# Performance work log

Measured on AMD Instinct MI355X. Metric: run time of the kernel, lower is better.

Reference implementation:

```python
import jax, jax.numpy as jnp
import numpy as np

L = 10      # LSTM layers
H = 128     # hidden size
ENC = 4096  # traffic_encoder_output_len
B = 8192    # batch
T = 12      # points_to_predict
NUM_MODES = 25


def setup_inputs() -> dict:
    key = jax.random.key(0)
    ks = jax.random.split(key, 10)
    s = 1.0 / np.sqrt(H)
    return {
        "backbone_encoded": jax.random.normal(ks[0], (B, ENC), jnp.float32),
        "fc_in_W": jax.random.normal(ks[1], (H, ENC), jnp.float32) / np.sqrt(ENC),
        "fc_in_b": jax.random.normal(ks[2], (H,), jnp.float32) * s,
        "Wih": jax.random.normal(ks[3], (L, 4 * H, H), jnp.float32) * s,
        "Whh": jax.random.normal(ks[4], (L, 4 * H, H), jnp.float32) * s,
        "bih": jax.random.normal(ks[5], (L, 4 * H), jnp.float32) * s,
        "bhh": jax.random.normal(ks[6], (L, 4 * H), jnp.float32) * s,
        "fc_out_W": jax.random.normal(ks[7], (3 * NUM_MODES, H), jnp.float32) * s,
        "fc_out_b": jax.random.normal(ks[8], (3 * NUM_MODES,), jnp.float32) * s,
        "points_to_predict": T,
    }


def _lstm_stack(x, Wih, Whh, bih, bhh):
    # x: [B, T, H]; PyTorch gate order: i, f, g, o
    def run_layer(x, l):
        def step(carry, xt):
            h, c = carry
            gates = xt @ Wih[l].T + h @ Whh[l].T + bih[l] + bhh[l]  # [B, 4H]
            i, f, g, o = jnp.split(gates, 4, axis=-1)
            c = jax.nn.sigmoid(f) * c + jax.nn.sigmoid(i) * jnp.tanh(g)
            h = jax.nn.sigmoid(o) * jnp.tanh(c)
            return (h, c), h
        b = x.shape[0]
        h0 = jnp.zeros((b, H), x.dtype)
        _, ys = jax.lax.scan(step, (h0, h0), jnp.swapaxes(x, 0, 1))  # [T, B, H]
        return jnp.swapaxes(ys, 0, 1)

    for l in range(L):
        x = run_layer(x, l)
    return x


def reference(backbone_encoded, fc_in_W, fc_in_b, Wih, Whh, bih, bhh,
              fc_out_W, fc_out_b, points_to_predict):
    enc = jax.nn.relu(backbone_encoded @ fc_in_W.T + fc_in_b)        # [B, H]
    x = jnp.repeat(enc[:, None, :], points_to_predict, axis=1)      # [B, T, H]
    y = _lstm_stack(x, Wih, Whh, bih, bhh)                           # [B, T, H]
    fc = y @ fc_out_W.T + fc_out_b                                   # [B, T, 75]
    b, t, _ = fc.shape
    # chunk(25, dim=channels) of consecutive pairs -> [B, 25, T, 2]
    predictions = fc[:, :, :50].reshape(b, t, NUM_MODES, 2).transpose(0, 2, 1, 3)
    probabilities = jax.nn.softmax(fc[:, -1, 50:], axis=-1)          # [B, 25]
    return predictions, probabilities
```

## Files before the change

kernel.cpp:

```cpp
#include <hip/hip_runtime.h>

typedef _Float16 h16;
typedef _Float16 h4 __attribute__((ext_vector_type(4)));
typedef _Float16 h8 __attribute__((ext_vector_type(8)));
typedef float f4 __attribute__((ext_vector_type(4)));

#define NB 8192
#define NENC 4096
#define NH 128
#define NL 10
#define NT 12
#define PAD 136

#define OFF_FCIN 0
#define SZ_FCIN (128*4096)
#define OFF_W (OFF_FCIN + SZ_FCIN)
#define SZ_W (10*2*512*128)
#define OFF_FCOUT (OFF_W + SZ_W)
#define SZ_FCOUT (80*128)
#define OFF_ENC (OFF_FCOUT + SZ_FCOUT)
#define SZ_ENC (8192*128)
#define OFF_GX0 (OFF_ENC + SZ_ENC)
#define SZ_GX0 (8192*512)
#define BYTE_BIAS ((OFF_GX0 + SZ_GX0)*2)

__device__ __forceinline__ float sigf(float x) {
  float e = __builtin_amdgcn_exp2f(-1.4426950408889634f * x);
  return __builtin_amdgcn_rcpf(1.0f + e);
}
__device__ __forceinline__ float tanhf_(float x) {
  float e = __builtin_amdgcn_exp2f(-2.8853900817779268f * x);
  return 2.0f * __builtin_amdgcn_rcpf(1.0f + e) - 1.0f;
}
__device__ __forceinline__ f4 splat4(float v) { f4 r; r[0]=v; r[1]=v; r[2]=v; r[3]=v; return r; }
__device__ __forceinline__ h8 cvt8(float4 a, float4 b) {
  h8 r; r[0]=(h16)a.x; r[1]=(h16)a.y; r[2]=(h16)a.z; r[3]=(h16)a.w;
  r[4]=(h16)b.x; r[5]=(h16)b.y; r[6]=(h16)b.z; r[7]=(h16)b.w; return r;
}

__global__ __launch_bounds__(256) void prep(const float* __restrict__ fcinW,
                                            const float* __restrict__ Wih,
                                            const float* __restrict__ Whh,
                                            const float* __restrict__ bih,
                                            const float* __restrict__ bhh,
                                            const float* __restrict__ fcoutW,
                                            h16* __restrict__ wsh,
                                            float* __restrict__ wbias) {
  int idx = blockIdx.x * 256 + threadIdx.x;
  if (idx < 65536) {
    int r = idx >> 9, k8 = idx & 511;
    const float* src = fcinW + r * 4096 + k8 * 8;
    h8 v = cvt8(*(const float4*)src, *(const float4*)(src + 4));
    *(h8*)(wsh + OFF_FCIN + (((r >> 4) * 512 + k8) * 128 + (r & 15) * 8)) = v;
  } else if (idx < 229376) {
    int rel = idx - 65536;
    int l = rel >> 14, rr = rel & 16383;
    int ssel = rr >> 13, rk8 = rr & 8191;
    int r = rk8 >> 4, k8 = rk8 & 15;
    const float* src = (ssel ? Whh : Wih) + l * 65536 + r * 128 + k8 * 8;
    h8 v = cvt8(*(const float4*)src, *(const float4*)(src + 4));
    *(h8*)(wsh + OFF_W + (l * 2 + ssel) * 65536 +
           (((r >> 4) * 16 + k8) * 128 + (r & 15) * 8)) = v;
  } else if (idx < 230656) {
    int rel = idx - 229376;
    int r = rel >> 4, k8 = rel & 15;
    h8 v;
    if (r < 75) {
      const float* src = fcoutW + r * 128 + k8 * 8;
      v = cvt8(*(const float4*)src, *(const float4*)(src + 4));
    } else {
      for (int j = 0; j < 8; ++j) v[j] = (h16)0.f;
    }
    *(h8*)(wsh + OFF_FCOUT + (((r >> 4) * 16 + k8) * 128 + (r & 15) * 8)) = v;
  } else if (idx < 235776) {
    int rel = idx - 230656;
    wbias[rel] = bih[rel] + bhh[rel];
  }
}

__global__ __launch_bounds__(256) void kin(const float* __restrict__ A,
                                           const float* __restrict__ bvec,
                                           h16* __restrict__ wsh) {
  const h16* Wp = wsh + OFF_FCIN;
  h16* ench = wsh + OFF_ENC;
  int tid = threadIdx.x;
  int w = tid >> 6, lane = tid & 63, s = lane & 15, q = lane >> 4;
  int m0 = blockIdx.x * 16;
  int c0 = w * 32 + s, c1 = c0 + 16;
  f4 acc0 = splat4(bvec[c0]);
  f4 acc1 = splat4(bvec[c1]);
  const float* arow = A + (size_t)(m0 + s) * NENC;
  const h16* wp0 = Wp + (w * 2 + 0) * (512 * 128) + s * 8;
  const h16* wp1 = Wp + (w * 2 + 1) * (512 * 128) + s * 8;
#pragma unroll 4
  for (int kb = 0; kb < 128; ++kb) {
    int k0 = kb * 32 + q * 8;
    float4 x0 = *(const float4*)(arow + k0);
    float4 x1 = *(const float4*)(arow + k0 + 4);
    h8 af = cvt8(x0, x1);
    h8 b0 = *(const h8*)(wp0 + (kb * 4 + q) * 128);
    h8 b1 = *(const h8*)(wp1 + (kb * 4 + q) * 128);
    acc0 = __builtin_amdgcn_mfma_f32_16x16x32_f16(af, b0, acc0, 0, 0, 0);
    acc1 = __builtin_amdgcn_mfma_f32_16x16x32_f16(af, b1, acc1, 0, 0, 0);
  }
#pragma unroll
  for (int r = 0; r < 4; ++r) {
    int b = m0 + q * 4 + r;
    float v0 = acc0[r]; v0 = v0 > 0.f ? v0 : 0.f;
    float v1 = acc1[r]; v1 = v1 > 0.f ? v1 : 0.f;
    ench[(size_t)b * NH + c0] = (h16)v0;
    ench[(size_t)b * NH + c1] = (h16)v1;
  }
}

__global__ __launch_bounds__(256) void kin2(h16* __restrict__ wsh,
                                            const float* __restrict__ wbias) {
  int tid = threadIdx.x;
  int w2 = tid >> 6, lane = tid & 63, s = lane & 15, q = lane >> 4;
  int bid = blockIdx.x;
  int lb = bid >> 3, mt = (bid >> 2) & 1, cg = bid & 3;
  const h16* ench = wsh + OFF_ENC;
  const h16* wih0 = wsh + OFF_W;
  h16* gx0 = wsh + OFF_GX0;
  const h16* arow = ench + (size_t)(lb * 32 + mt * 16 + s) * NH;
  h8 ax[4];
#pragma unroll
  for (int kt = 0; kt < 4; ++kt) ax[kt] = *(const h8*)(arow + kt * 32 + q * 8);
#pragma unroll
  for (int ti = 0; ti < 2; ++ti) {
    int W = w2 * 2 + ti;
    int rb = cg * 8 + W;
    f4 acc = splat4(wbias[cg * 128 + W * 16 + s]);
#pragma unroll
    for (int kt = 0; kt < 4; ++kt) {
      h8 b = *(const h8*)(wih0 + (rb * 16 + kt * 4 + q) * 128 + s * 8);
      acc = __builtin_amdgcn_mfma_f32_16x16x32_f16(ax[kt], b, acc, 0, 0, 0);
    }
    h4 st; st[0] = (h16)acc[0]; st[1] = (h16)acc[1]; st[2] = (h16)acc[2]; st[3] = (h16)acc[3];
    *(h4*)(gx0 + ((((size_t)lb * 8 + W) * 8 + cg * 2 + mt) * 64 + lane) * 4) = st;
  }
}

__global__ __launch_bounds__(512, 2) void lstm(h16* __restrict__ wsh,
                                               const float* __restrict__ wbias,
                                               const float* __restrict__ fcoutb,
                                               float* __restrict__ out) {
  __shared__ h16 ring[13][32][PAD];
  __shared__ float probst[32 * 26];
  int tid = threadIdx.x;
  int w = tid >> 6, lane = tid & 63, s = lane & 15, q = lane >> 4;
  int brow = blockIdx.x * 32;
  h8 wx[4][4], wh[4][4];
  float bb[4];
  float c[2][4];

  {
    const h16* whh = wsh + OFF_W + 65536;
#pragma unroll
    for (int g = 0; g < 4; ++g)
#pragma unroll
      for (int kt = 0; kt < 4; ++kt)
        wh[g][kt] = *(const h8*)(whh + (((g * 8 + w) * 16 + kt * 4 + q) * 128) + s * 8);
    f4 gx[4][2];
    const h16* gxp = wsh + OFF_GX0 + ((size_t)blockIdx.x * 8 + w) * 8 * 256 + (size_t)lane * 4;
#pragma unroll
    for (int g = 0; g < 4; ++g)
#pragma unroll
      for (int mt = 0; mt < 2; ++mt) {
        h4 v = *(const h4*)(gxp + (g * 2 + mt) * 256);
        f4 a; a[0] = (float)v[0]; a[1] = (float)v[1]; a[2] = (float)v[2]; a[3] = (float)v[3];
        gx[g][mt] = a;
      }
#pragma unroll
    for (int mt = 0; mt < 2; ++mt)
#pragma unroll
      for (int r = 0; r < 4; ++r) c[mt][r] = 0.f;
    for (int t = 0; t < NT; ++t) {
      __syncthreads();
      int rw = t + 11; if (rw >= 13) rw -= 13;
      int rh = t + 10; if (rh >= 13) rh -= 13;
      f4 acc[4][2];
#pragma unroll
      for (int g = 0; g < 4; ++g)
#pragma unroll
        for (int mt = 0; mt < 2; ++mt) acc[g][mt] = gx[g][mt];
      if (t > 0) {
#pragma unroll
        for (int mt = 0; mt < 2; ++mt) {
          h8 ah[4];
#pragma unroll
          for (int kt = 0; kt < 4; ++kt)
            ah[kt] = *(const h8*)&ring[rh][mt * 16 + s][kt * 32 + q * 8];
#pragma unroll
          for (int g = 0; g < 4; ++g)
#pragma unroll
            for (int kt = 0; kt < 4; ++kt)
              acc[g][mt] = __builtin_amdgcn_mfma_f32_16x16x32_f16(ah[kt], wh[g][kt], acc[g][mt], 0, 0, 0);
        }
      }
#pragma unroll
      for (int mt = 0; mt < 2; ++mt)
#pragma unroll
        for (int r = 0; r < 4; ++r) {
          float iv = acc[0][mt][r], fv = acc[1][mt][r];
          float gv = acc[2][mt][r], ov = acc[3][mt][r];
          float cc = sigf(fv) * c[mt][r] + sigf(iv) * tanhf_(gv);
          c[mt][r] = cc;
          ring[rw][mt * 16 + q * 4 + r][w * 16 + s] = (h16)(sigf(ov) * tanhf_(cc));
        }
    }
  }
  for (int l = 1; l < NL; ++l) {
    const h16* wih = wsh + OFF_W + (size_t)(l * 2) * 65536;
    const h16* whh = wih + 65536;
#pragma unroll
    for (int g = 0; g < 4; ++g) {
#pragma unroll
      for (int kt = 0; kt < 4; ++kt) {
        int off = (((g * 8 + w) * 16 + kt * 4 + q) * 128) + s * 8;
        wx[g][kt] = *(const h8*)(wih + off);
        wh[g][kt] = *(const h8*)(whh + off);
      }
      bb[g] = wbias[l * 512 + g * 128 + w * 16 + s];
    }
#pragma unroll
    for (int mt = 0; mt < 2; ++mt)
#pragma unroll
      for (int r = 0; r < 4; ++r) c[mt][r] = 0.f;
    int base = 12 - l;
    for (int t = 0; t < NT; ++t) {
      __syncthreads();
      int rr = t + base; if (rr >= 13) rr -= 13;
      int rw = rr - 1; if (rw < 0) rw += 13;
      int rh = rw - 1; if (rh < 0) rh += 13;
      f4 acc[4][2];
#pragma unroll
      for (int g = 0; g < 4; ++g)
#pragma unroll
        for (int mt = 0; mt < 2; ++mt) acc[g][mt] = splat4(bb[g]);
#pragma unroll
      for (int mt = 0; mt < 2; ++mt) {
        h8 ax[4];
#pragma unroll
        for (int kt = 0; kt < 4; ++kt)
          ax[kt] = *(const h8*)&ring[rr][mt * 16 + s][kt * 32 + q * 8];
#pragma unroll
        for (int g = 0; g < 4; ++g)
#pragma unroll
          for (int kt = 0; kt < 4; ++kt)
            acc[g][mt] = __builtin_amdgcn_mfma_f32_16x16x32_f16(ax[kt], wx[g][kt], acc[g][mt], 0, 0, 0);
      }
      if (t > 0) {
#pragma unroll
        for (int mt = 0; mt < 2; ++mt) {
          h8 ah[4];
#pragma unroll
          for (int kt = 0; kt < 4; ++kt)
            ah[kt] = *(const h8*)&ring[rh][mt * 16 + s][kt * 32 + q * 8];
#pragma unroll
          for (int g = 0; g < 4; ++g)
#pragma unroll
            for (int kt = 0; kt < 4; ++kt)
              acc[g][mt] = __builtin_amdgcn_mfma_f32_16x16x32_f16(ah[kt], wh[g][kt], acc[g][mt], 0, 0, 0);
        }
      }
#pragma unroll
      for (int mt = 0; mt < 2; ++mt)
#pragma unroll
        for (int r = 0; r < 4; ++r) {
          float iv = acc[0][mt][r], fv = acc[1][mt][r];
          float gv = acc[2][mt][r], ov = acc[3][mt][r];
          float cc = sigf(fv) * c[mt][r] + sigf(iv) * tanhf_(gv);
          c[mt][r] = cc;
          ring[rw][mt * 16 + q * 4 + r][w * 16 + s] = (h16)(sigf(ov) * tanhf_(cc));
        }
    }
  }
  __syncthreads();
  h8 wo[5][4];
  float bo[5];
  const h16* fco = wsh + OFF_FCOUT;
#pragma unroll
  for (int nt = 0; nt < 5; ++nt) {
#pragma unroll
    for (int kt = 0; kt < 4; ++kt)
      wo[nt][kt] = *(const h8*)(fco + (nt * 16 + kt * 4 + q) * 128 + s * 8);
    int col = nt * 16 + s;
    bo[nt] = (col < 75) ? fcoutb[col] : 0.f;
  }
  int tcount = (w < 4) ? 2 : 1;
  for (int ti = 0; ti < tcount; ++ti) {
    int t = w + ti * 8;
    int sl = t + 2; if (sl >= 13) sl -= 13;
#pragma unroll
    for (int mt = 0; mt < 2; ++mt) {
      h8 ax[4];
#pragma unroll
      for (int kt = 0; kt < 4; ++kt)
        ax[kt] = *(const h8*)&ring[sl][mt * 16 + s][kt * 32 + q * 8];
#pragma unroll
      for (int nt = 0; nt < 5; ++nt) {
        f4 a = splat4(bo[nt]);
#pragma unroll
        for (int kt = 0; kt < 4; ++kt)
          a = __builtin_amdgcn_mfma_f32_16x16x32_f16(ax[kt], wo[nt][kt], a, 0, 0, 0);
        int col = nt * 16 + s;
#pragma unroll
        for (int r = 0; r < 4; ++r) {
          int row = mt * 16 + q * 4 + r;
          int b = brow + row;
          float v = a[r];
          if (col < 50)
            out[(size_t)b * 600 + (col >> 1) * 24 + t * 2 + (col & 1)] = v;
          if (t == 11 && col >= 50 && col < 75)
            probst[row * 26 + (col - 50)] = v;
        }
      }
    }
  }
  __syncthreads();
  if (tid < 32) {
    float vals[25];
    float m = -1e30f;
#pragma unroll
    for (int j = 0; j < 25; ++j) { vals[j] = probst[tid * 26 + j]; m = vals[j] > m ? vals[j] : m; }
    float sum = 0.f;
#pragma unroll
    for (int j = 0; j < 25; ++j) {
      float e = __builtin_amdgcn_exp2f((vals[j] - m) * 1.4426950408889634f);
      vals[j] = e; sum += e;
    }
    float rs = 1.0f / sum;
    size_t pb = (size_t)4915200 + (size_t)(brow + tid) * 25;
#pragma unroll
    for (int j = 0; j < 25; ++j) out[pb + j] = vals[j] * rs;
  }
}

extern "C" void kernel_launch(void* const* d_in, const int* in_sizes, int n_in,
                              void* d_out, int out_size, void* d_ws, size_t ws_size,
                              hipStream_t stream) {
  const float* backbone = (const float*)d_in[0];
  const float* fcinW    = (const float*)d_in[1];
  const float* fcinb    = (const float*)d_in[2];
  const float* Wih      = (const float*)d_in[3];
  const float* Whh      = (const float*)d_in[4];
  const float* bih      = (const float*)d_in[5];
  const float* bhh      = (const float*)d_in[6];
  const float* fcoutW   = (const float*)d_in[7];
  const float* fcoutb   = (const float*)d_in[8];
  h16* wsh = (h16*)d_ws;
  float* wbias = (float*)((char*)d_ws + BYTE_BIAS);

  prep<<<922, 256, 0, stream>>>(fcinW, Wih, Whh, bih, bhh, fcoutW, wsh, wbias);
  kin<<<512, 256, 0, stream>>>(backbone, fcinb, wsh);
  kin2<<<2048, 256, 0, stream>>>(wsh, wbias);
  lstm<<<256, 512, 0, stream>>>(wsh, wbias, fcoutb, (float*)d_out);
}
```

Before: 514.7 us.

## Fuse layer-0 input projection and bias/fc_out prep into LSTM kernel

Removes the separate kin2 kernel that precomputed the layer-0 input gates into a workspace buffer; the LSTM kernel now computes them directly from the encoder output with MFMA. Bias summation and fc_out weight conversion move from prep into the LSTM kernel, and the gate activations are rewritten to share reciprocals (sigmoid*tanh merged into one rcp). The LDS ring padding also changes. This drops a kernel launch and the global round-trip of the gate buffer, at the cost of extra registers and redundant per-block weight conversion.

New measurement: 534.3 us. +3.8%, slower.

```diff
diff --git a/kernel.cpp b/kernel.cpp
--- a/kernel.cpp
+++ b/kernel.cpp
@@ -1,7 +1,6 @@
 #include <hip/hip_runtime.h>
 
 typedef _Float16 h16;
-typedef _Float16 h4 __attribute__((ext_vector_type(4)));
 typedef _Float16 h8 __attribute__((ext_vector_type(8)));
 typedef float f4 __attribute__((ext_vector_type(4)));
 
@@ -10,28 +9,17 @@
 #define NH 128
 #define NL 10
 #define NT 12
-#define PAD 136
+#define PAD 138
 
 #define OFF_FCIN 0
 #define SZ_FCIN (128*4096)
 #define OFF_W (OFF_FCIN + SZ_FCIN)
 #define SZ_W (10*2*512*128)
-#define OFF_FCOUT (OFF_W + SZ_W)
-#define SZ_FCOUT (80*128)
-#define OFF_ENC (OFF_FCOUT + SZ_FCOUT)
+#define OFF_ENC (OFF_W + SZ_W)
 #define SZ_ENC (8192*128)
-#define OFF_GX0 (OFF_ENC + SZ_ENC)
-#define SZ_GX0 (8192*512)
-#define BYTE_BIAS ((OFF_GX0 + SZ_GX0)*2)
-
-__device__ __forceinline__ float sigf(float x) {
-  float e = __builtin_amdgcn_exp2f(-1.4426950408889634f * x);
-  return __builtin_amdgcn_rcpf(1.0f + e);
-}
-__device__ __forceinline__ float tanhf_(float x) {
-  float e = __builtin_amdgcn_exp2f(-2.8853900817779268f * x);
-  return 2.0f * __builtin_amdgcn_rcpf(1.0f + e) - 1.0f;
-}
+
+#define KLOG2 1.4426950408889634f
+
 __device__ __forceinline__ f4 splat4(float v) { f4 r; r[0]=v; r[1]=v; r[2]=v; r[3]=v; return r; }
 __device__ __forceinline__ h8 cvt8(float4 a, float4 b) {
   h8 r; r[0]=(h16)a.x; r[1]=(h16)a.y; r[2]=(h16)a.z; r[3]=(h16)a.w;
@@ -41,11 +29,7 @@
 __global__ __launch_bounds__(256) void prep(const float* __restrict__ fcinW,
                                             const float* __restrict__ Wih,
                                             const float* __restrict__ Whh,
-                                            const float* __restrict__ bih,
-                                            const float* __restrict__ bhh,
-                                            const float* __restrict__ fcoutW,
-                                            h16* __restrict__ wsh,
-                                            float* __restrict__ wbias) {
+                                            h16* __restrict__ wsh) {
   int idx = blockIdx.x * 256 + threadIdx.x;
   if (idx < 65536) {
     int r = idx >> 9, k8 = idx & 511;
@@ -61,20 +45,6 @@
     h8 v = cvt8(*(const float4*)src, *(const float4*)(src + 4));
     *(h8*)(wsh + OFF_W + (l * 2 + ssel) * 65536 +
            (((r >> 4) * 16 + k8) * 128 + (r & 15) * 8)) = v;
-  } else if (idx < 230656) {
-    int rel = idx - 229376;
-    int r = rel >> 4, k8 = rel & 15;
-    h8 v;
-    if (r < 75) {
-      const float* src = fcoutW + r * 128 + k8 * 8;
-      v = cvt8(*(const float4*)src, *(const float4*)(src + 4));
-    } else {
-      for (int j = 0; j < 8; ++j) v[j] = (h16)0.f;
-    }
-    *(h8*)(wsh + OFF_FCOUT + (((r >> 4) * 16 + k8) * 128 + (r & 15) * 8)) = v;
-  } else if (idx < 235776) {
-    int rel = idx - 230656;
-    wbias[rel] = bih[rel] + bhh[rel];
   }
 }
 
@@ -113,36 +83,10 @@
   }
 }
 
-__global__ __launch_bounds__(256) void kin2(h16* __restrict__ wsh,
-                                            const float* __restrict__ wbias) {
-  int tid = threadIdx.x;
-  int w2 = tid >> 6, lane = tid & 63, s = lane & 15, q = lane >> 4;
-  int bid = blockIdx.x;
-  int lb = bid >> 3, mt = (bid >> 2) & 1, cg = bid & 3;
-  const h16* ench = wsh + OFF_ENC;
-  const h16* wih0 = wsh + OFF_W;
-  h16* gx0 = wsh + OFF_GX0;
-  const h16* arow = ench + (size_t)(lb * 32 + mt * 16 + s) * NH;
-  h8 ax[4];
-#pragma unroll
-  for (int kt = 0; kt < 4; ++kt) ax[kt] = *(const h8*)(arow + kt * 32 + q * 8);
-#pragma unroll
-  for (int ti = 0; ti < 2; ++ti) {
-    int W = w2 * 2 + ti;
-    int rb = cg * 8 + W;
-    f4 acc = splat4(wbias[cg * 128 + W * 16 + s]);
-#pragma unroll
-    for (int kt = 0; kt < 4; ++kt) {
-      h8 b = *(const h8*)(wih0 + (rb * 16 + kt * 4 + q) * 128 + s * 8);
-      acc = __builtin_amdgcn_mfma_f32_16x16x32_f16(ax[kt], b, acc, 0, 0, 0);
-    }
-    h4 st; st[0] = (h16)acc[0]; st[1] = (h16)acc[1]; st[2] = (h16)acc[2]; st[3] = (h16)acc[3];
-    *(h4*)(gx0 + ((((size_t)lb * 8 + W) * 8 + cg * 2 + mt) * 64 + lane) * 4) = st;
-  }
-}
-
 __global__ __launch_bounds__(512, 2) void lstm(h16* __restrict__ wsh,
-                                               const float* __restrict__ wbias,
+                                               const float* __restrict__ bih,
+                                               const float* __restrict__ bhh,
+                                               const float* __restrict__ fcoutW,
                                                const float* __restrict__ fcoutb,
                                                float* __restrict__ out) {
   __shared__ h16 ring[13][32][PAD];
@@ -150,27 +94,41 @@
   int tid = threadIdx.x;
   int w = tid >> 6, lane = tid & 63, s = lane & 15, q = lane >> 4;
   int brow = blockIdx.x * 32;
+  const h16* ench = wsh + OFF_ENC;
   h8 wx[4][4], wh[4][4];
-  float bb[4];
   float c[2][4];
 
+  f4 gx[4][2];
   {
-    const h16* whh = wsh + OFF_W + 65536;
-#pragma unroll
-    for (int g = 0; g < 4; ++g)
+    const h16* wih0 = wsh + OFF_W;
+    const h16* whh0 = wih0 + 65536;
+#pragma unroll
+    for (int g = 0; g < 4; ++g) {
+#pragma unroll
+      for (int kt = 0; kt < 4; ++kt) {
+        int off = (((g * 8 + w) * 16 + kt * 4 + q) * 128) + s * 8;
+        wx[g][kt] = *(const h8*)(wih0 + off);
+        wh[g][kt] = *(const h8*)(whh0 + off);
+      }
+      int bcol = g * 128 + w * 16 + s;
+      float bb = bih[bcol] + bhh[bcol];
+#pragma unroll
+      for (int mt = 0; mt < 2; ++mt) gx[g][mt] = splat4(bb);
+    }
+#pragma unroll
+    for (int mt = 0; mt < 2; ++mt) {
+      h8 ax[4];
 #pragma unroll
       for (int kt = 0; kt < 4; ++kt)
-        wh[g][kt] = *(const h8*)(whh + (((g * 8 + w) * 16 + kt * 4 + q) * 128) + s * 8);
-    f4 gx[4][2];
-    const h16* gxp = wsh + OFF_GX0 + ((size_t)blockIdx.x * 8 + w) * 8 * 256 + (size_t)lane * 4;
-#pragma unroll
-    for (int g = 0; g < 4; ++g)
-#pragma unroll
-      for (int mt = 0; mt < 2; ++mt) {
-        h4 v = *(const h4*)(gxp + (g * 2 + mt) * 256);
-        f4 a; a[0] = (float)v[0]; a[1] = (float)v[1]; a[2] = (float)v[2]; a[3] = (float)v[3];
-        gx[g][mt] = a;
-      }
+        ax[kt] = *(const h8*)(ench + (size_t)(brow + mt * 16 + s) * NH + kt * 32 + q * 8);
+#pragma unroll
+      for (int g = 0; g < 4; ++g)
+#pragma unroll
+        for (int kt = 0; kt < 4; ++kt)
+          gx[g][mt] = __builtin_amdgcn_mfma_f32_16x16x32_f16(ax[kt], wx[g][kt], gx[g][mt], 0, 0, 0);
+    }
+  }
+  {
 #pragma unroll
     for (int mt = 0; mt < 2; ++mt)
 #pragma unroll
@@ -203,16 +161,24 @@
 #pragma unroll
         for (int r = 0; r < 4; ++r) {
           float iv = acc[0][mt][r], fv = acc[1][mt][r];
-          float gv = acc[2][mt][r], ov = acc[3][mt][r];
-          float cc = sigf(fv) * c[mt][r] + sigf(iv) * tanhf_(gv);
+          float gv = fmaxf(acc[2][mt][r], -30.f), ov = acc[3][mt][r];
+          float ui = __builtin_amdgcn_exp2f(-KLOG2 * iv);
+          float ug = __builtin_amdgcn_exp2f(-2.f * KLOG2 * gv);
+          float uf = __builtin_amdgcn_exp2f(-KLOG2 * fv);
+          float ig = (1.f - ug) * __builtin_amdgcn_rcpf((1.f + ui) * (1.f + ug));
+          float cc = c[mt][r] * __builtin_amdgcn_rcpf(1.f + uf) + ig;
           c[mt][r] = cc;
-          ring[rw][mt * 16 + q * 4 + r][w * 16 + s] = (h16)(sigf(ov) * tanhf_(cc));
+          float uo = __builtin_amdgcn_exp2f(-KLOG2 * ov);
+          float uc = __builtin_amdgcn_exp2f(-2.f * KLOG2 * cc);
+          float hv = (1.f - uc) * __builtin_amdgcn_rcpf((1.f + uo) * (1.f + uc));
+          ring[rw][mt * 16 + q * 4 + r][w * 16 + s] = (h16)hv;
         }
     }
   }
   for (int l = 1; l < NL; ++l) {
     const h16* wih = wsh + OFF_W + (size_t)(l * 2) * 65536;
     const h16* whh = wih + 65536;
+    float bb[4];
 #pragma unroll
     for (int g = 0; g < 4; ++g) {
 #pragma unroll
@@ -221,7 +187,8 @@
         wx[g][kt] = *(const h8*)(wih + off);
         wh[g][kt] = *(const h8*)(whh + off);
       }
-      bb[g] = wbias[l * 512 + g * 128 + w * 16 + s];
+      int bcol = l * 512 + g * 128 + w * 16 + s;
+      bb[g] = bih[bcol] + bhh[bcol];
     }
 #pragma unroll
     for (int mt = 0; mt < 2; ++mt)
@@ -269,24 +236,37 @@
 #pragma unroll
         for (int r = 0; r < 4; ++r) {
           float iv = acc[0][mt][r], fv = acc[1][mt][r];
-          float gv = acc[2][mt][r], ov = acc[3][mt][r];
-          float cc = sigf(fv) * c[mt][r] + sigf(iv) * tanhf_(gv);
+          float gv = fmaxf(acc[2][mt][r], -30.f), ov = acc[3][mt][r];
+          float ui = __builtin_amdgcn_exp2f(-KLOG2 * iv);
+          float ug = __builtin_amdgcn_exp2f(-2.f * KLOG2 * gv);
+          float uf = __builtin_amdgcn_exp2f(-KLOG2 * fv);
+          float ig = (1.f - ug) * __builtin_amdgcn_rcpf((1.f + ui) * (1.f + ug));
+          float cc = c[mt][r] * __builtin_amdgcn_rcpf(1.f + uf) + ig;
           c[mt][r] = cc;
-          ring[rw][mt * 16 + q * 4 + r][w * 16 + s] = (h16)(sigf(ov) * tanhf_(cc));
+          float uo = __builtin_amdgcn_exp2f(-KLOG2 * ov);
+          float uc = __builtin_amdgcn_exp2f(-2.f * KLOG2 * cc);
+          float hv = (1.f - uc) * __builtin_amdgcn_rcpf((1.f + uo) * (1.f + uc));
+          ring[rw][mt * 16 + q * 4 + r][w * 16 + s] = (h16)hv;
         }
     }
   }
   __syncthreads();
   h8 wo[5][4];
   float bo[5];
-  const h16* fco = wsh + OFF_FCOUT;
 #pragma unroll
   for (int nt = 0; nt < 5; ++nt) {
-#pragma unroll
-    for (int kt = 0; kt < 4; ++kt)
-      wo[nt][kt] = *(const h8*)(fco + (nt * 16 + kt * 4 + q) * 128 + s * 8);
-    int col = nt * 16 + s;
-    bo[nt] = (col < 75) ? fcoutb[col] : 0.f;
+    int row = nt * 16 + s;
+    bool ok = row < 75;
+#pragma unroll
+    for (int kt = 0; kt < 4; ++kt) {
+      const float* p = ok ? (fcoutW + row * 128 + kt * 32 + q * 8) : fcoutW;
+      float4 x0 = *(const float4*)p;
+      float4 x1 = *(const float4*)(p + 4);
+      h8 v = cvt8(x0, x1);
+      if (!ok) for (int j = 0; j < 8; ++j) v[j] = (h16)0.f;
+      wo[nt][kt] = v;
+    }
+    bo[nt] = ok ? fcoutb[row] : 0.f;
   }
   int tcount = (w < 4) ? 2 : 1;
   for (int ti = 0; ti < tcount; ++ti) {
@@ -327,7 +307,7 @@
     float sum = 0.f;
 #pragma unroll
     for (int j = 0; j < 25; ++j) {
-      float e = __builtin_amdgcn_exp2f((vals[j] - m) * 1.4426950408889634f);
+      float e = __builtin_amdgcn_exp2f((vals[j] - m) * KLOG2);
       vals[j] = e; sum += e;
     }
     float rs = 1.0f / sum;
@@ -350,10 +330,8 @@
   const float* fcoutW   = (const float*)d_in[7];
   const float* fcoutb   = (const float*)d_in[8];
   h16* wsh = (h16*)d_ws;
-  float* wbias = (float*)((char*)d_ws + BYTE_BIAS);
-
-  prep<<<922, 256, 0, stream>>>(fcinW, Wih, Whh, bih, bhh, fcoutW, wsh, wbias);
+
+  prep<<<896, 256, 0, stream>>>(fcinW, Wih, Whh, wsh);
   kin<<<512, 256, 0, stream>>>(backbone, fcinb, wsh);
-  kin2<<<2048, 256, 0, stream>>>(wsh, wbias);
-  lstm<<<256, 512, 0, stream>>>(wsh, wbias, fcoutb, (float*)d_out);
-}
+  lstm<<<256, 512, 0, stream>>>(wsh, bih, bhh, fcoutW, fcoutb, (float*)d_out);
+}
```
